# Optimization experiments

Hardware: AMD Instinct MI355X
Metric: run time of the kernel (lower is better)

## Reference

```python
import jax, jax.numpy as jnp
import numpy as np

EPS = 1e-5
NH = 4          # num_heads
DH = 128        # head_dim
ALPHA = 1.0 / float(np.sqrt(DH))


def _ln(x, w, b):
    m = x.mean(-1, keepdims=True)
    v = x.var(-1, keepdims=True)
    return (x - m) * jax.lax.rsqrt(v + EPS) * w + b


def setup_inputs() -> dict:
    key = jax.random.key(0)
    ks = jax.random.split(key, 8)
    D = 512                 # hidden_size
    U = 4 * NH * DH         # uvqk linear out = 2048
    B, S, H = 32, 256, 2048  # batch, new tokens/seq, history len/seq
    NT = B * S              # 8192 flattened jagged tokens
    layer_input = jax.random.normal(ks[0], (NT, D), dtype=jnp.float32)
    hist_k = jax.random.normal(ks[1], (B, H, NH, DH), dtype=jnp.float32) * 0.1
    hist_v = jax.random.normal(ks[2], (B, H, NH, DH), dtype=jnp.float32) * 0.1
    # torch init: uniform(-0.5, 0.5); scaled down for numerical sanity
    W_uvqk = (jax.random.uniform(ks[3], (D, U), dtype=jnp.float32) - 0.5) * 0.1
    b_uvqk = (jax.random.uniform(ks[4], (U,), dtype=jnp.float32) - 0.5) * 0.1
    ln_in_w = jnp.ones((D,), jnp.float32)
    ln_in_b = jnp.zeros((D,), jnp.float32)
    ln_out_w = jnp.ones((NH * DH,), jnp.float32)
    ln_out_b = jnp.zeros((NH * DH,), jnp.float32)
    W_proj = jax.random.normal(ks[5], (NH * DH, D), dtype=jnp.float32) * 0.05
    return {
        "layer_input": layer_input, "hist_k": hist_k, "hist_v": hist_v,
        "ln_in_w": ln_in_w, "ln_in_b": ln_in_b,
        "W_uvqk": W_uvqk, "b_uvqk": b_uvqk,
        "ln_out_w": ln_out_w, "ln_out_b": ln_out_b, "W_proj": W_proj,
    }


def reference(layer_input, hist_k, hist_v, ln_in_w, ln_in_b,
              W_uvqk, b_uvqk, ln_out_w, ln_out_b, W_proj):
    B, H, nh, dh = hist_k.shape
    NT, D = layer_input.shape
    S = NT // B
    dspl = nh * dh
    # ln -> linear+bias -> silu (fused u,v,q,k projection)
    x = _ln(layer_input, ln_in_w, ln_in_b)
    uvqk = jax.nn.silu(x @ W_uvqk + b_uvqk)
    u, v, q, k = jnp.split(uvqk, 4, axis=-1)   # order: user, value, query, key
    q = q.reshape(B, S, nh, dh)
    k = k.reshape(B, S, nh, dh)
    v = v.reshape(B, S, nh, dh)
    # paged KV-cache append == concat new k,v after history
    K = jnp.concatenate([hist_k, k], axis=1)   # [B, T, nh, dh], T = H+S
    V = jnp.concatenate([hist_v, v], axis=1)
    T = H + S
    # HSTU varlen attention: silu(alpha * q k^T) with causal delta-q mask,
    # query i sits at global position H+i and may attend to kv pos <= H+i
    scores = jnp.einsum('bsnd,btnd->bnst', q, K) * ALPHA
    mask = jnp.arange(T)[None, :] <= (H + jnp.arange(S))[:, None]  # [S, T]
    p = jnp.where(mask[None, None], jax.nn.silu(scores), 0.0)
    attn = jnp.einsum('bnst,btnd->bsnd', p, V).reshape(NT, dspl)
    # gated output LN, projection, residual
    parallel = u * _ln(attn, ln_out_w, ln_out_b)
    return parallel @ W_proj + layer_input
```

## Files before the change

kernel.cpp:

```cpp
#include <hip/hip_runtime.h>
#include <hip/hip_bf16.h>


typedef __attribute__((ext_vector_type(8))) short v8s;
typedef __attribute__((ext_vector_type(4))) float v4f;
typedef __attribute__((ext_vector_type(4))) unsigned short v4us;
typedef __attribute__((ext_vector_type(4))) unsigned int v4u;

#define D_HID 512
#define U_DIM 2048
#define NHEAD 4
#define DHEAD 128
#define BATCH 32
#define SEQ   256
#define HIST  2048
#define NTOK  8192
#define ALPHA_ 0.08838834764831845f
#define EPS_   1e-5f

__device__ __forceinline__ unsigned short f2bf(float f) {
  unsigned int u = __float_as_uint(f);
  u += 0x7FFFu + ((u >> 16) & 1u);
  return (unsigned short)(u >> 16);
}
__device__ __forceinline__ float bf2f(unsigned short s) {
  return __uint_as_float(((unsigned int)s) << 16);
}
__device__ __forceinline__ float siluf(float x) {
  return x * __builtin_amdgcn_rcpf(1.0f + __expf(-x));
}
__device__ __forceinline__ unsigned int cvtpk(float lo, float hi) {
  __hip_bfloat162 h = __float22bfloat162_rn(make_float2(lo, hi));
  union { __hip_bfloat162 h; unsigned int u; } cv; cv.h = h;
  return cv.u;
}

__global__ __launch_bounds__(256) void ln_in_kernel(
    const float* __restrict__ x, const float* __restrict__ w,
    const float* __restrict__ b, unsigned short* __restrict__ out)
{
  int wid = threadIdx.x >> 6, lane = threadIdx.x & 63;
  int row = blockIdx.x * 4 + wid;
  const float* xr = x + (size_t)row * D_HID + lane * 8;
  float4 a0 = *(const float4*)xr;
  float4 a1 = *(const float4*)(xr + 4);
  float v[8] = {a0.x, a0.y, a0.z, a0.w, a1.x, a1.y, a1.z, a1.w};
  float s = 0.f, s2 = 0.f;
#pragma unroll
  for (int j = 0; j < 8; ++j) { s += v[j]; s2 += v[j] * v[j]; }
#pragma unroll
  for (int m = 1; m < 64; m <<= 1) { s += __shfl_xor(s, m, 64); s2 += __shfl_xor(s2, m, 64); }
  float mean = s * (1.f / D_HID);
  float var  = s2 * (1.f / D_HID) - mean * mean;
  float rstd = rsqrtf(var + EPS_);
  const float* wp = w + lane * 8; const float* bp = b + lane * 8;
  float4 w0 = *(const float4*)wp, w1 = *(const float4*)(wp + 4);
  float4 b0 = *(const float4*)bp, b1 = *(const float4*)(bp + 4);
  float wv[8] = {w0.x, w0.y, w0.z, w0.w, w1.x, w1.y, w1.z, w1.w};
  float bv[8] = {b0.x, b0.y, b0.z, b0.w, b1.x, b1.y, b1.z, b1.w};
  v8s o;
#pragma unroll
  for (int j = 0; j < 8; ++j) o[j] = (short)f2bf((v[j] - mean) * rstd * wv[j] + bv[j]);
  *(v8s*)(out + (size_t)row * D_HID + lane * 8) = o;
}

__global__ __launch_bounds__(256) void gated_ln_kernel(
    const float* __restrict__ attn0, const float* __restrict__ attn1,
    const unsigned short* __restrict__ uvqk,
    const float* __restrict__ w, const float* __restrict__ b,
    unsigned short* __restrict__ par)
{
  int wid = threadIdx.x >> 6, lane = threadIdx.x & 63;
  int row = blockIdx.x * 4 + wid;
  size_t off = (size_t)row * D_HID + lane * 8;
  float4 x0 = *(const float4*)(attn0 + off), x1 = *(const float4*)(attn0 + off + 4);
  float4 y0 = *(const float4*)(attn1 + off), y1 = *(const float4*)(attn1 + off + 4);
  float v[8] = {x0.x + y0.x, x0.y + y0.y, x0.z + y0.z, x0.w + y0.w,
                x1.x + y1.x, x1.y + y1.y, x1.z + y1.z, x1.w + y1.w};
  float s = 0.f, s2 = 0.f;
#pragma unroll
  for (int j = 0; j < 8; ++j) { s += v[j]; s2 += v[j] * v[j]; }
#pragma unroll
  for (int m = 1; m < 64; m <<= 1) { s += __shfl_xor(s, m, 64); s2 += __shfl_xor(s2, m, 64); }
  float mean = s * (1.f / D_HID);
  float var  = s2 * (1.f / D_HID) - mean * mean;
  float rstd = rsqrtf(var + EPS_);
  const float* wp = w + lane * 8; const float* bp = b + lane * 8;
  float4 w0 = *(const float4*)wp, w1 = *(const float4*)(wp + 4);
  float4 b0 = *(const float4*)bp, b1 = *(const float4*)(bp + 4);
  float wv[8] = {w0.x, w0.y, w0.z, w0.w, w1.x, w1.y, w1.z, w1.w};
  float bv[8] = {b0.x, b0.y, b0.z, b0.w, b1.x, b1.y, b1.z, b1.w};
  v8s uv = *(const v8s*)(uvqk + (size_t)row * U_DIM + lane * 8);
  v8s o;
#pragma unroll
  for (int j = 0; j < 8; ++j) {
    float u = bf2f((unsigned short)uv[j]);
    o[j] = (short)f2bf(u * ((v[j] - mean) * rstd * wv[j] + bv[j]));
  }
  *(v8s*)(par + (size_t)row * D_HID + lane * 8) = o;
}

__global__ __launch_bounds__(256) void transpose_w_kernel(
    const float* __restrict__ in, unsigned short* __restrict__ out, int R, int C)
{
  __shared__ float tile[32][33];
  int c0 = blockIdx.x * 32, r0 = blockIdx.y * 32;
  int tr = threadIdx.x >> 3;
  int tc = (threadIdx.x & 7) * 4;
  float4 vv = *(const float4*)(in + (size_t)(r0 + tr) * C + c0 + tc);
  tile[tr][tc + 0] = vv.x; tile[tr][tc + 1] = vv.y;
  tile[tr][tc + 2] = vv.z; tile[tr][tc + 3] = vv.w;
  __syncthreads();
  v4us o;
#pragma unroll
  for (int j = 0; j < 4; ++j) o[j] = f2bf(tile[tc + j][tr]);
  *(v4us*)(out + (size_t)(c0 + tr) * R + r0 + tc) = o;
}

template <int EPI>
__global__ __launch_bounds__(256) void gemm_kernel(
    const unsigned short* __restrict__ A, const unsigned short* __restrict__ Bt,
    int K, int N,
    const float* __restrict__ bias, const float* __restrict__ resid,
    unsigned short* __restrict__ outb, float* __restrict__ outf)
{
  __shared__ unsigned short Al[128 * 40];
  __shared__ unsigned short Bl[128 * 40];
  int m0 = blockIdx.x * 128, n0 = blockIdx.y * 128;
  int tid = threadIdx.x, lane = tid & 63, wid = tid >> 6;
  int wr = wid >> 1, wc = wid & 1;
  int lr = lane & 15, lg = lane >> 4;

  v4f acc[4][4];
#pragma unroll
  for (int i = 0; i < 4; ++i)
#pragma unroll
    for (int j = 0; j < 4; ++j) acc[i][j] = (v4f){0.f, 0.f, 0.f, 0.f};

  int srow = tid >> 1;
  int sc   = (tid & 1) * 16;
  const unsigned short* ga = A  + (size_t)(m0 + srow) * K + sc;
  const unsigned short* gb = Bt + (size_t)(n0 + srow) * K + sc;

  for (int k0 = 0; k0 < K; k0 += 32) {
    v8s a0 = *(const v8s*)(ga + k0);
    v8s a1 = *(const v8s*)(ga + k0 + 8);
    v8s b0 = *(const v8s*)(gb + k0);
    v8s b1 = *(const v8s*)(gb + k0 + 8);
    *(v8s*)&Al[srow * 40 + sc]     = a0;
    *(v8s*)&Al[srow * 40 + sc + 8] = a1;
    *(v8s*)&Bl[srow * 40 + sc]     = b0;
    *(v8s*)&Bl[srow * 40 + sc + 8] = b1;
    __syncthreads();
    v8s af[4], bf[4];
#pragma unroll
    for (int mt = 0; mt < 4; ++mt) af[mt] = *(const v8s*)&Al[(wr * 64 + mt * 16 + lr) * 40 + lg * 8];
#pragma unroll
    for (int nt = 0; nt < 4; ++nt) bf[nt] = *(const v8s*)&Bl[(wc * 64 + nt * 16 + lr) * 40 + lg * 8];
#pragma unroll
    for (int mt = 0; mt < 4; ++mt)
#pragma unroll
      for (int nt = 0; nt < 4; ++nt)
        acc[mt][nt] = __builtin_amdgcn_mfma_f32_16x16x32_bf16(af[mt], bf[nt], acc[mt][nt], 0, 0, 0);
    __syncthreads();
  }

#pragma unroll
  for (int nt = 0; nt < 4; ++nt) {
    int col = n0 + wc * 64 + nt * 16 + lr;
    float bi = 0.f;
    if constexpr (EPI == 0) bi = bias[col];
#pragma unroll
    for (int mt = 0; mt < 4; ++mt) {
      int row0 = m0 + wr * 64 + mt * 16 + lg * 4;
#pragma unroll
      for (int r = 0; r < 4; ++r) {
        float xv = acc[mt][nt][r];
        if constexpr (EPI == 0) {
          float rv = siluf(xv + bi);
          if ((unsigned)(col - 2 * D_HID) < (unsigned)D_HID) rv *= ALPHA_;
          outb[(size_t)(row0 + r) * N + col] = f2bf(rv);
        } else {
          outf[(size_t)(row0 + r) * N + col] = xv + resid[(size_t)(row0 + r) * N + col];
        }
      }
    }
  }
}

__global__ __launch_bounds__(512, 2) void attn_kernel(
    const float* __restrict__ histK, const float* __restrict__ histV,
    const unsigned short* __restrict__ uvqk, float* __restrict__ attn_out)
{
  __shared__ __align__(16) unsigned short Kl[2 * 64 * 136];
  __shared__ __align__(16) unsigned short Vt[2 * 128 * 72];
  __shared__ __align__(16) unsigned short Pl[8 * 32 * 72];

  int bid = blockIdx.x;
  int q   = bid >> 7;
  int b   = (bid >> 2) & 31;
  int n   = bid & 3;
  int tbase0 = q * 1152;
  const int NT = 18;

  int tid = threadIdx.x, lane = tid & 63, w = tid >> 6;
  int lr = lane & 15, lg = lane >> 4;

  v8s qf[2][4];
#pragma unroll
  for (int sb = 0; sb < 2; ++sb) {
    const unsigned short* qp = uvqk + (size_t)(b * SEQ + w * 32 + sb * 16 + lr) * U_DIM
                               + 2 * D_HID + n * DHEAD + lg * 8;
#pragma unroll
    for (int c = 0; c < 4; ++c) qf[sb][c] = *(const v8s*)(qp + c * 32);
  }

  v4f oacc[2][8];
#pragma unroll
  for (int sb = 0; sb < 2; ++sb)
#pragma unroll
    for (int dt = 0; dt < 8; ++dt) oacc[sb][dt] = (v4f){0.f, 0.f, 0.f, 0.f};

  int m     = tid & 15;
  int std0  = m * 8;
  int strow = tid >> 4;
  int vkey  = 8 * (m & 7);

  const float* kbase = histK + (((size_t)b * HIST) * NHEAD + n) * DHEAD + std0;
  const float* vbase = histV + (((size_t)b * HIST) * NHEAD + n) * DHEAD + std0;
  const unsigned short* nkbase = uvqk + (size_t)(b * SEQ) * U_DIM + 3 * D_HID + n * DHEAD + std0;
  const unsigned short* nvbase = uvqk + (size_t)(b * SEQ) * U_DIM + 1 * D_HID + n * DHEAD + std0;

  float4 hx[2][4];
  v8s    nx[2][2];
  int isnew_r = 0;

  auto stage_load = [&](int kt) {
    int tb = tbase0 + kt * 64;
    if (tb < HIST) {
      isnew_r = 0;
#pragma unroll
      for (int p = 0; p < 2; ++p) {
        unsigned off = ((unsigned)(tb + 2 * strow + p)) << 9;
        hx[p][0] = *(const float4*)(kbase + off);
        hx[p][1] = *(const float4*)(kbase + off + 4);
        hx[p][2] = *(const float4*)(vbase + off);
        hx[p][3] = *(const float4*)(vbase + off + 4);
      }
    } else {
      isnew_r = 1;
#pragma unroll
      for (int p = 0; p < 2; ++p) {
        unsigned off = ((unsigned)(tb - HIST + 2 * strow + p)) << 11;
        nx[p][0] = *(const v8s*)(nkbase + off);
        nx[p][1] = *(const v8s*)(nvbase + off);
      }
    }
  };

  auto stage_store = [&](int buf) {
    unsigned short* Kb = &Kl[buf * (64 * 136)];
    unsigned short* Vb = &Vt[buf * (128 * 72)];
    int t0 = 2 * strow;
    if (!isnew_r) {
#pragma unroll
      for (int p = 0; p < 2; ++p) {
        v4u kp;
        kp[0] = cvtpk(hx[p][0].x, hx[p][0].y);
        kp[1] = cvtpk(hx[p][0].z, hx[p][0].w);
        kp[2] = cvtpk(hx[p][1].x, hx[p][1].y);
        kp[3] = cvtpk(hx[p][1].z, hx[p][1].w);
        *(v4u*)&Kb[(t0 + p) * 136 + std0] = kp;
      }
      float v0[8] = {hx[0][2].x, hx[0][2].y, hx[0][2].z, hx[0][2].w,
                     hx[0][3].x, hx[0][3].y, hx[0][3].z, hx[0][3].w};
      float v1[8] = {hx[1][2].x, hx[1][2].y, hx[1][2].z, hx[1][2].w,
                     hx[1][3].x, hx[1][3].y, hx[1][3].z, hx[1][3].w};
#pragma unroll
      for (int j = 0; j < 8; ++j) {
        int d = std0 + j;
        *(unsigned int*)&Vb[d * 72 + (t0 ^ vkey)] = cvtpk(v0[j], v1[j]);
      }
    } else {
#pragma unroll
      for (int p = 0; p < 2; ++p) *(v8s*)&Kb[(t0 + p) * 136 + std0] = nx[p][0];
#pragma unroll
      for (int j = 0; j < 8; ++j) {
        int d = std0 + j;
        unsigned int pk = (unsigned int)(unsigned short)nx[0][1][j]
                        | ((unsigned int)(unsigned short)nx[1][1][j] << 16);
        *(unsigned int*)&Vb[d * 72 + (t0 ^ vkey)] = pk;
      }
    }
  };

  stage_load(0);
  stage_store(0);
  stage_load(1);
  __syncthreads();

  unsigned short* Plw = &Pl[w * 32 * 72];

  for (int kt = 0; kt < NT; ++kt) {
    int cur = kt & 1;
    if (kt + 1 < NT) stage_store(cur ^ 1);
    if (kt + 2 < NT) stage_load(kt + 2);

    int tb = tbase0 + kt * 64;
    bool masked = (tb >= HIST);
    const unsigned short* Kb = &Kl[cur * (64 * 136)];
    const unsigned short* Vb = &Vt[cur * (128 * 72)];

    __builtin_amdgcn_s_setprio(1);
#pragma unroll
    for (int tt = 0; tt < 4; ++tt) {
      v8s kf[4];
#pragma unroll
      for (int c = 0; c < 4; ++c)
        kf[c] = *(const v8s*)&Kb[(tt * 16 + lr) * 136 + c * 32 + lg * 8];
#pragma unroll
      for (int sb = 0; sb < 2; ++sb) {
        v4f sa = (v4f){0.f, 0.f, 0.f, 0.f};
#pragma unroll
        for (int c = 0; c < 4; ++c)
          sa = __builtin_amdgcn_mfma_f32_16x16x32_bf16(kf[c], qf[sb][c], sa, 0, 0, 0);
        int s  = w * 32 + sb * 16 + lr;
        int t0 = tb + tt * 16 + lg * 4;
#pragma unroll
        for (int rp = 0; rp < 2; ++rp) {
          float p0 = siluf(sa[rp * 2]);
          float p1 = siluf(sa[rp * 2 + 1]);
          if (masked) {
            if (t0 + rp * 2     - HIST > s) p0 = 0.f;
            if (t0 + rp * 2 + 1 - HIST > s) p1 = 0.f;
          }
          *(unsigned int*)&Plw[(sb * 16 + lr) * 72 + tt * 16 + lg * 4 + rp * 2] =
              cvtpk(p0, p1);
        }
      }
    }

#pragma unroll
    for (int c = 0; c < 2; ++c) {
      v8s pa[2];
#pragma unroll
      for (int sb = 0; sb < 2; ++sb)
        pa[sb] = *(const v8s*)&Plw[(sb * 16 + lr) * 72 + c * 32 + lg * 8];
#pragma unroll
      for (int dt = 0; dt < 8; ++dt) {
        int d = dt * 16 + lr;
        int rkey = 8 * ((2 * dt + (lr >> 3)) & 7);
        v8s vf = *(const v8s*)&Vb[d * 72 + ((c * 32 + lg * 8) ^ rkey)];
#pragma unroll
        for (int sb = 0; sb < 2; ++sb)
          oacc[sb][dt] = __builtin_amdgcn_mfma_f32_16x16x32_bf16(vf, pa[sb], oacc[sb][dt], 0, 0, 0);
      }
    }
    __builtin_amdgcn_s_setprio(0);

    if (kt + 1 < NT) __syncthreads();
  }

#pragma unroll
  for (int sb = 0; sb < 2; ++sb) {
    float* op = attn_out + (size_t)q * ((size_t)NTOK * D_HID)
              + (size_t)(b * SEQ + w * 32 + sb * 16 + lr) * D_HID
              + n * DHEAD + lg * 4;
#pragma unroll
    for (int dt = 0; dt < 8; ++dt) {
      float4 o4 = make_float4(oacc[sb][dt][0], oacc[sb][dt][1],
                              oacc[sb][dt][2], oacc[sb][dt][3]);
      *(float4*)(op + dt * 16) = o4;
    }
  }
}

extern "C" void kernel_launch(void* const* d_in, const int* in_sizes, int n_in,
                              void* d_out, int out_size, void* d_ws, size_t ws_size,
                              hipStream_t stream)
{
  (void)in_sizes; (void)n_in; (void)out_size; (void)ws_size;

  const float* layer_input = (const float*)d_in[0];
  const float* hist_k   = (const float*)d_in[1];
  const float* hist_v   = (const float*)d_in[2];
  const float* ln_in_w  = (const float*)d_in[3];
  const float* ln_in_b  = (const float*)d_in[4];
  const float* W_uvqk   = (const float*)d_in[5];
  const float* b_uvqk   = (const float*)d_in[6];
  const float* ln_out_w = (const float*)d_in[7];
  const float* ln_out_b = (const float*)d_in[8];
  const float* W_proj   = (const float*)d_in[9];
  float* out = (float*)d_out;

  char* ws = (char*)d_ws;
  unsigned short* uvqk    = (unsigned short*)(ws);
  float*          attn0   = (float*)         (ws + (32u << 20));
  float*          attn1   = (float*)         (ws + (48u << 20));
  unsigned short* x_bf    = (unsigned short*)(ws + (48u << 20));
  unsigned short* par     = (unsigned short*)(ws + (64u << 20));
  unsigned short* wt_uvqk = (unsigned short*)(ws + (72u << 20));
  unsigned short* wt_proj = (unsigned short*)(ws + (74u << 20));

  ln_in_kernel<<<dim3(2048), dim3(256), 0, stream>>>(layer_input, ln_in_w, ln_in_b, x_bf);
  transpose_w_kernel<<<dim3(64, 16), dim3(256), 0, stream>>>(W_uvqk, wt_uvqk, 512, 2048);
  transpose_w_kernel<<<dim3(16, 16), dim3(256), 0, stream>>>(W_proj, wt_proj, 512, 512);
  gemm_kernel<0><<<dim3(64, 16), dim3(256), 0, stream>>>(x_bf, wt_uvqk, 512, 2048,
                                                         b_uvqk, nullptr, uvqk, nullptr);
  attn_kernel<<<dim3(256), dim3(512), 0, stream>>>(hist_k, hist_v, uvqk, attn0);
  gated_ln_kernel<<<dim3(2048), dim3(256), 0, stream>>>(attn0, attn1, uvqk, ln_out_w, ln_out_b, par);
  gemm_kernel<1><<<dim3(64, 4), dim3(256), 0, stream>>>(par, wt_proj, 512, 512,
                                                        nullptr, layer_input, nullptr, out);
}
```

Measured before the change: 173.2 us.

## Switch attention to 32x32x16 MFMA with register-resident P via lane shuffles

New measurement: 170.3 us. Within noise of the previous version (-1.7%).

```diff
diff --git a/kernel.cpp b/kernel.cpp
--- a/kernel.cpp
+++ b/kernel.cpp
@@ -4,6 +4,7 @@
 
 typedef __attribute__((ext_vector_type(8))) short v8s;
 typedef __attribute__((ext_vector_type(4))) float v4f;
+typedef __attribute__((ext_vector_type(16))) float v16f;
 typedef __attribute__((ext_vector_type(4))) unsigned short v4us;
 typedef __attribute__((ext_vector_type(4))) unsigned int v4u;
 
@@ -192,9 +193,8 @@
     const float* __restrict__ histK, const float* __restrict__ histV,
     const unsigned short* __restrict__ uvqk, float* __restrict__ attn_out)
 {
-  __shared__ __align__(16) unsigned short Kl[2 * 64 * 136];
-  __shared__ __align__(16) unsigned short Vt[2 * 128 * 72];
-  __shared__ __align__(16) unsigned short Pl[8 * 32 * 72];
+  __shared__ __align__(16) unsigned short Kl[2 * 64 * 128];
+  __shared__ __align__(16) unsigned short Vt[2 * 128 * 64];
 
   int bid = blockIdx.x;
   int q   = bid >> 7;
@@ -204,27 +204,28 @@
   const int NT = 18;
 
   int tid = threadIdx.x, lane = tid & 63, w = tid >> 6;
-  int lr = lane & 15, lg = lane >> 4;
-
-  v8s qf[2][4];
-#pragma unroll
-  for (int sb = 0; sb < 2; ++sb) {
-    const unsigned short* qp = uvqk + (size_t)(b * SEQ + w * 32 + sb * 16 + lr) * U_DIM
-                               + 2 * D_HID + n * DHEAD + lg * 8;
-#pragma unroll
-    for (int c = 0; c < 4; ++c) qf[sb][c] = *(const v8s*)(qp + c * 32);
-  }
-
-  v4f oacc[2][8];
-#pragma unroll
-  for (int sb = 0; sb < 2; ++sb)
-#pragma unroll
-    for (int dt = 0; dt < 8; ++dt) oacc[sb][dt] = (v4f){0.f, 0.f, 0.f, 0.f};
+  int l5 = lane & 31;
+  int hi = lane >> 5;
+  int hi8 = hi * 8;
+  int sq = w * 32 + l5;
+
+  v8s qf[8];
+  {
+    const unsigned short* qp = uvqk + (size_t)(b * SEQ + sq) * U_DIM
+                               + 2 * D_HID + n * DHEAD + hi8;
+#pragma unroll
+    for (int ks = 0; ks < 8; ++ks) qf[ks] = *(const v8s*)(qp + ks * 16);
+  }
+
+  v16f oacc[4];
+#pragma unroll
+  for (int i = 0; i < 4; ++i)
+#pragma unroll
+    for (int r = 0; r < 16; ++r) oacc[i][r] = 0.f;
 
   int m     = tid & 15;
   int std0  = m * 8;
   int strow = tid >> 4;
-  int vkey  = 8 * (m & 7);
 
   const float* kbase = histK + (((size_t)b * HIST) * NHEAD + n) * DHEAD + std0;
   const float* vbase = histV + (((size_t)b * HIST) * NHEAD + n) * DHEAD + std0;
@@ -259,18 +260,19 @@
   };
 
   auto stage_store = [&](int buf) {
-    unsigned short* Kb = &Kl[buf * (64 * 136)];
-    unsigned short* Vb = &Vt[buf * (128 * 72)];
+    unsigned short* Kb = &Kl[buf * 8192];
+    unsigned short* Vb = &Vt[buf * 8192];
     int t0 = 2 * strow;
     if (!isnew_r) {
 #pragma unroll
       for (int p = 0; p < 2; ++p) {
+        int t = t0 + p;
         v4u kp;
         kp[0] = cvtpk(hx[p][0].x, hx[p][0].y);
         kp[1] = cvtpk(hx[p][0].z, hx[p][0].w);
         kp[2] = cvtpk(hx[p][1].x, hx[p][1].y);
         kp[3] = cvtpk(hx[p][1].z, hx[p][1].w);
-        *(v4u*)&Kb[(t0 + p) * 136 + std0] = kp;
+        *(v4u*)&Kb[t * 128 + (std0 ^ ((t & 7) << 3))] = kp;
       }
       float v0[8] = {hx[0][2].x, hx[0][2].y, hx[0][2].z, hx[0][2].w,
                      hx[0][3].x, hx[0][3].y, hx[0][3].z, hx[0][3].w};
@@ -279,17 +281,22 @@
 #pragma unroll
       for (int j = 0; j < 8; ++j) {
         int d = std0 + j;
-        *(unsigned int*)&Vb[d * 72 + (t0 ^ vkey)] = cvtpk(v0[j], v1[j]);
+        int col = t0 ^ ((((d >> 3) ^ d) & 7) << 3);
+        *(unsigned int*)&Vb[d * 64 + col] = cvtpk(v0[j], v1[j]);
       }
     } else {
 #pragma unroll
-      for (int p = 0; p < 2; ++p) *(v8s*)&Kb[(t0 + p) * 136 + std0] = nx[p][0];
+      for (int p = 0; p < 2; ++p) {
+        int t = t0 + p;
+        *(v8s*)&Kb[t * 128 + (std0 ^ ((t & 7) << 3))] = nx[p][0];
+      }
 #pragma unroll
       for (int j = 0; j < 8; ++j) {
         int d = std0 + j;
+        int col = t0 ^ ((((d >> 3) ^ d) & 7) << 3);
         unsigned int pk = (unsigned int)(unsigned short)nx[0][1][j]
                         | ((unsigned int)(unsigned short)nx[1][1][j] << 16);
-        *(unsigned int*)&Vb[d * 72 + (t0 ^ vkey)] = pk;
+        *(unsigned int*)&Vb[d * 64 + col] = pk;
       }
     }
   };
@@ -299,8 +306,6 @@
   stage_load(1);
   __syncthreads();
 
-  unsigned short* Plw = &Pl[w * 32 * 72];
-
   for (int kt = 0; kt < NT; ++kt) {
     int cur = kt & 1;
     if (kt + 1 < NT) stage_store(cur ^ 1);
@@ -308,52 +313,66 @@
 
     int tb = tbase0 + kt * 64;
     bool masked = (tb >= HIST);
-    const unsigned short* Kb = &Kl[cur * (64 * 136)];
-    const unsigned short* Vb = &Vt[cur * (128 * 72)];
+    const unsigned short* Kb = &Kl[cur * 8192];
+    const unsigned short* Vb = &Vt[cur * 8192];
 
     __builtin_amdgcn_s_setprio(1);
-#pragma unroll
-    for (int tt = 0; tt < 4; ++tt) {
-      v8s kf[4];
-#pragma unroll
-      for (int c = 0; c < 4; ++c)
-        kf[c] = *(const v8s*)&Kb[(tt * 16 + lr) * 136 + c * 32 + lg * 8];
-#pragma unroll
-      for (int sb = 0; sb < 2; ++sb) {
-        v4f sa = (v4f){0.f, 0.f, 0.f, 0.f};
-#pragma unroll
-        for (int c = 0; c < 4; ++c)
-          sa = __builtin_amdgcn_mfma_f32_16x16x32_bf16(kf[c], qf[sb][c], sa, 0, 0, 0);
-        int s  = w * 32 + sb * 16 + lr;
-        int t0 = tb + tt * 16 + lg * 4;
-#pragma unroll
-        for (int rp = 0; rp < 2; ++rp) {
-          float p0 = siluf(sa[rp * 2]);
-          float p1 = siluf(sa[rp * 2 + 1]);
-          if (masked) {
-            if (t0 + rp * 2     - HIST > s) p0 = 0.f;
-            if (t0 + rp * 2 + 1 - HIST > s) p1 = 0.f;
-          }
-          *(unsigned int*)&Plw[(sb * 16 + lr) * 72 + tt * 16 + lg * 4 + rp * 2] =
-              cvtpk(p0, p1);
+
+    v8s pb[4];
+#pragma unroll
+    for (int tt = 0; tt < 2; ++tt) {
+      v16f sa;
+#pragma unroll
+      for (int r = 0; r < 16; ++r) sa[r] = 0.f;
+      int trow = tt * 32 + l5;
+      int kx = (trow & 7) << 3;
+      int krow = trow * 128;
+#pragma unroll
+      for (int ks = 0; ks < 8; ++ks) {
+        v8s kf = *(const v8s*)&Kb[krow + ((ks * 16 + hi8) ^ kx)];
+        sa = __builtin_amdgcn_mfma_f32_32x32x16_bf16(kf, qf[ks], sa, 0, 0, 0);
+      }
+      unsigned e[8];
+      if (masked) {
+        int thr = sq - (tb - HIST) - tt * 32 - 4 * hi;
+#pragma unroll
+        for (int i = 0; i < 8; ++i) {
+          int r0 = 2 * i, r1 = 2 * i + 1;
+          int tl0 = (r0 & 3) + 8 * (r0 >> 2);
+          int tl1 = (r1 & 3) + 8 * (r1 >> 2);
+          float p0 = (tl0 <= thr) ? siluf(sa[r0]) : 0.f;
+          float p1 = (tl1 <= thr) ? siluf(sa[r1]) : 0.f;
+          e[i] = cvtpk(p0, p1);
         }
-      }
-    }
-
-#pragma unroll
-    for (int c = 0; c < 2; ++c) {
-      v8s pa[2];
-#pragma unroll
-      for (int sb = 0; sb < 2; ++sb)
-        pa[sb] = *(const v8s*)&Plw[(sb * 16 + lr) * 72 + c * 32 + lg * 8];
-#pragma unroll
-      for (int dt = 0; dt < 8; ++dt) {
-        int d = dt * 16 + lr;
-        int rkey = 8 * ((2 * dt + (lr >> 3)) & 7);
-        v8s vf = *(const v8s*)&Vb[d * 72 + ((c * 32 + lg * 8) ^ rkey)];
-#pragma unroll
-        for (int sb = 0; sb < 2; ++sb)
-          oacc[sb][dt] = __builtin_amdgcn_mfma_f32_16x16x32_bf16(vf, pa[sb], oacc[sb][dt], 0, 0, 0);
+      } else {
+#pragma unroll
+        for (int i = 0; i < 8; ++i) e[i] = cvtpk(siluf(sa[2 * i]), siluf(sa[2 * i + 1]));
+      }
+#pragma unroll
+      for (int h = 0; h < 2; ++h) {
+        unsigned a0 = e[h * 4 + 0], a1 = e[h * 4 + 1];
+        unsigned b0 = e[h * 4 + 2], b1 = e[h * 4 + 3];
+        unsigned sa0 = (unsigned)__shfl_xor((int)a0, 32, 64);
+        unsigned sa1 = (unsigned)__shfl_xor((int)a1, 32, 64);
+        unsigned sb0 = (unsigned)__shfl_xor((int)b0, 32, 64);
+        unsigned sb1 = (unsigned)__shfl_xor((int)b1, 32, 64);
+        union { unsigned u[4]; v8s s; } U;
+        U.u[0] = hi ? sb0 : a0;
+        U.u[1] = hi ? sb1 : a1;
+        U.u[2] = hi ? b0 : sa0;
+        U.u[3] = hi ? b1 : sa1;
+        pb[tt * 2 + h] = U.s;
+      }
+    }
+
+#pragma unroll
+    for (int ks = 0; ks < 4; ++ks) {
+#pragma unroll
+      for (int dt4 = 0; dt4 < 4; ++dt4) {
+        int d = dt4 * 32 + l5;
+        int col = (ks * 16 + hi8) ^ ((((d >> 3) ^ d) & 7) << 3);
+        v8s vf = *(const v8s*)&Vb[d * 64 + col];
+        oacc[dt4] = __builtin_amdgcn_mfma_f32_32x32x16_bf16(vf, pb[ks], oacc[dt4], 0, 0, 0);
       }
     }
     __builtin_amdgcn_s_setprio(0);
@@ -361,16 +380,17 @@
     if (kt + 1 < NT) __syncthreads();
   }
 
-#pragma unroll
-  for (int sb = 0; sb < 2; ++sb) {
+  {
     float* op = attn_out + (size_t)q * ((size_t)NTOK * D_HID)
-              + (size_t)(b * SEQ + w * 32 + sb * 16 + lr) * D_HID
-              + n * DHEAD + lg * 4;
-#pragma unroll
-    for (int dt = 0; dt < 8; ++dt) {
-      float4 o4 = make_float4(oacc[sb][dt][0], oacc[sb][dt][1],
-                              oacc[sb][dt][2], oacc[sb][dt][3]);
-      *(float4*)(op + dt * 16) = o4;
+              + (size_t)(b * SEQ + sq) * D_HID + n * DHEAD + 4 * hi;
+#pragma unroll
+    for (int dt4 = 0; dt4 < 4; ++dt4) {
+#pragma unroll
+      for (int g = 0; g < 4; ++g) {
+        float4 o4 = make_float4(oacc[dt4][4 * g + 0], oacc[dt4][4 * g + 1],
+                                oacc[dt4][4 * g + 2], oacc[dt4][4 * g + 3]);
+        *(float4*)(op + dt4 * 32 + 8 * g) = o4;
+      }
     }
   }
 }
```
